# Optimization experiments

Measured on AMD Instinct MI355X. Metric: run time of the kernel, lower is better.

The kernel has to match this reference:

```python
import jax, jax.numpy as jnp
import numpy as np

# Each of the 16 soft binary logic functions f_i(a,b) used by difflogic's
# LogicLayer is multilinear in {1, a, b, a*b}. Row i gives coefficients
# (c1, ca, cb, cab) such that f_i(a,b) = c1 + ca*a + cb*b + cab*a*b.
LOGIC_COEFFS = jnp.array([
    [0.,  0.,  0.,  0.],   # 0: False
    [0.,  0.,  0.,  1.],   # 1: a AND b
    [0.,  1.,  0., -1.],   # 2: a AND NOT b
    [0.,  1.,  0.,  0.],   # 3: a
    [0.,  0.,  1., -1.],   # 4: NOT a AND b
    [0.,  0.,  1.,  0.],   # 5: b
    [0.,  1.,  1., -2.],   # 6: a XOR b
    [0.,  1.,  1., -1.],   # 7: a OR b
    [1., -1., -1.,  1.],   # 8: NOT (a OR b)
    [1., -1., -1.,  2.],   # 9: NOT (a XOR b)
    [1.,  0., -1.,  0.],   # 10: NOT b
    [1.,  0., -1.,  1.],   # 11: a OR NOT b
    [1., -1.,  0.,  0.],   # 12: NOT a
    [1., -1.,  0.,  1.],   # 13: NOT a OR b
    [1.,  0.,  0., -1.],   # 14: NOT (a AND b)
    [1.,  0.,  0.,  0.],   # 15: True
], dtype=jnp.float32)

BATCH = 8192
K = 4096          # num_neurons
L = 6             # num_layers (1 layer 2->K, then L-1 layers K->K)
CLASS_COUNT = 2
TAU = 1.0


def _logic_layer(h, idx, w):
    # h: [B, in_dim], idx: [2, K] int, w: [K, 16]
    a = jnp.take(h, idx[0], axis=1)             # [B, K]
    b = jnp.take(h, idx[1], axis=1)             # [B, K]
    c = jax.nn.softmax(w, axis=-1) @ LOGIC_COEFFS  # [K, 4]
    return c[:, 0] + c[:, 1] * a + c[:, 2] * b + c[:, 3] * (a * b)


def setup_inputs() -> dict:
    key = jax.random.key(0)
    k1, k2, k3, k4, k5 = jax.random.split(key, 5)
    x = jax.random.normal(k1, (BATCH, 2), dtype=jnp.float32)
    w0 = jax.random.normal(k2, (K, 16), dtype=jnp.float32)
    ws = jax.random.normal(k3, (L - 1, K, 16), dtype=jnp.float32)
    idx0 = jax.random.randint(k4, (2, K), 0, 2, dtype=jnp.int32)
    idxs = jax.random.randint(k5, (L - 1, 2, K), 0, K, dtype=jnp.int32)
    return {"x": x, "w0": w0, "ws": ws, "idx0": idx0, "idxs": idxs}


def reference(x, w0, ws, idx0, idxs):
    h = (x > 0.0).astype(jnp.float32)            # binarize input
    h = _logic_layer(h, idx0, w0)                # 2 -> K

    def step(h, wi):
        w, idx = wi
        return _logic_layer(h, idx, w), None

    h, _ = jax.lax.scan(step, h, (ws, idxs))     # (L-1) layers K -> K
    B, Kd = h.shape
    # GroupSum(class_count=2, tau=1.0)
    return h.reshape(B, CLASS_COUNT, Kd // CLASS_COUNT).sum(-1) / TAU
```

## Files before the change

kernel.cpp:

```cpp
#include <hip/hip_runtime.h>

#define KN    4096
#define LTOT  6
#define BATCH 8192
#define NT    1024
#define NITER (KN / NT)
#define NPAT  4

#if __has_builtin(__builtin_amdgcn_cvt_pk_u8_f32)
#define CVT_PK_U8(o, r, enc) __builtin_amdgcn_cvt_pk_u8_f32((o), (r), (enc))
#else
#define CVT_PK_U8(o, r, enc) ((enc) | ((unsigned)(int)(o) << (8 * (r))))
#endif

__global__ __launch_bounds__(256) void pack_kernel(const float* __restrict__ w0,
                                                   const float* __restrict__ ws,
                                                   const int* __restrict__ idx0,
                                                   const int* __restrict__ idxs,
                                                   uint2* __restrict__ pk) {
    const float TAB[16][4] = {
        {0.f, 0.f, 0.f, 0.f}, {0.f, 0.f, 0.f, 1.f}, {0.f, 1.f, 0.f,-1.f}, {0.f, 1.f, 0.f, 0.f},
        {0.f, 0.f, 1.f,-1.f}, {0.f, 0.f, 1.f, 0.f}, {0.f, 1.f, 1.f,-2.f}, {0.f, 1.f, 1.f,-1.f},
        {1.f,-1.f,-1.f, 1.f}, {1.f,-1.f,-1.f, 2.f}, {1.f, 0.f,-1.f, 0.f}, {1.f, 0.f,-1.f, 1.f},
        {1.f,-1.f, 0.f, 0.f}, {1.f,-1.f, 0.f, 1.f}, {1.f, 0.f, 0.f,-1.f}, {1.f, 0.f, 0.f, 0.f}
    };
    int gid = blockIdx.x * 256 + threadIdx.x;
    if (gid >= LTOT * KN) return;
    int l = gid >> 12;
    int k = gid & (KN - 1);
    const float* w = (l == 0) ? (w0 + k * 16) : (ws + ((size_t)((l - 1) * KN + k) << 4));
    float wv[16];
    float m = -1e30f;
#pragma unroll
    for (int j = 0; j < 16; ++j) { wv[j] = w[j]; m = fmaxf(m, wv[j]); }
    float s = 0.f;
#pragma unroll
    for (int j = 0; j < 16; ++j) { wv[j] = __expf(wv[j] - m); s += wv[j]; }
    float inv = 1.0f / s;
    float c0 = 0.f, c1 = 0.f, c2 = 0.f, c3 = 0.f;
#pragma unroll
    for (int j = 0; j < 16; ++j) {
        c0 += wv[j] * TAB[j][0];
        c1 += wv[j] * TAB[j][1];
        c2 += wv[j] * TAB[j][2];
        c3 += wv[j] * TAB[j][3];
    }
    c0 *= inv; c1 *= inv; c2 *= inv; c3 *= inv;

    float w00 = c0;
    float w01 = c0 + c2;
    float w10 = c0 + c1;
    float w11 = c0 + c1 + c2 + c3;
    unsigned q00 = (unsigned)min(255, max(0, (int)(w00 * 255.f + 0.5f)));
    unsigned q01 = (unsigned)min(255, max(0, (int)(w01 * 255.f + 0.5f)));
    unsigned q10 = (unsigned)min(255, max(0, (int)(w10 * 255.f + 0.5f)));
    unsigned q11 = (unsigned)min(255, max(0, (int)(w11 * 255.f + 0.5f)));

    int ia, ib;
    if (l == 0) { ia = idx0[k];                            ib = idx0[KN + k]; }
    else        { ia = idxs[(size_t)(l - 1) * 2 * KN + k]; ib = idxs[(size_t)(l - 1) * 2 * KN + KN + k]; }

    uint2 e;
    e.x = ((unsigned)ia * 4u) | (((unsigned)ib * 4u) << 16);
    e.y = q00 | (q01 << 8) | (q10 << 16) | (q11 << 24);
    pk[gid] = e;
}

#define COEFFS(CW)                                                              \
    float W00 = (float)((CW) & 0xffu);                                          \
    float W01 = (float)(((CW) >> 8) & 0xffu);                                   \
    float W10 = (float)(((CW) >> 16) & 0xffu);                                  \
    float W11 = (float)((CW) >> 24);                                            \
    float C1  = W00 + 0.5f;                                                     \
    float CA  = (W10 - W00) * (1.f / 255.f);                                    \
    float CB  = (W01 - W00) * (1.f / 255.f);                                    \
    float CAB = (W11 - W10 - W01 + W00) * (1.f / 65025.f);

__global__ __launch_bounds__(NT) void net_kernel(const uint2* __restrict__ pk,
                                                 float* __restrict__ table) {
    __shared__ unsigned hbuf[2][KN];
    __shared__ float red[NT / 64][8];

    const int t = threadIdx.x;

    uint2 op[LTOT][NITER];
#pragma unroll
    for (int l = 0; l < LTOT; ++l)
#pragma unroll
        for (int i = 0; i < NITER; ++i)
            op[l][i] = pk[(size_t)l * KN + i * NT + t];

#pragma unroll
    for (int l = 0; l < LTOT; ++l)
#pragma unroll
        for (int i = 0; i < NITER; ++i)
            asm volatile("" :: "v"(op[l][i].x), "v"(op[l][i].y));

#pragma unroll
    for (int i = 0; i < NITER; ++i) {
        int k = t + i * NT;
        unsigned px = op[0][i].x;
        unsigned av = (px & 0xffffu) ? 0xFFFF0000u : 0xFF00FF00u;
        unsigned bv = (px >> 16)     ? 0xFFFF0000u : 0xFF00FF00u;
        COEFFS(op[0][i].y);
        unsigned enc = 0;
#pragma unroll
        for (int r = 0; r < 4; ++r) {
            float af = (float)((av >> (8 * r)) & 0xffu);
            float bf = (float)((bv >> (8 * r)) & 0xffu);
            float o = fmaf(fmaf(CAB, bf, CA), af, fmaf(CB, bf, C1));
            enc = CVT_PK_U8(o, r, enc);
        }
        hbuf[0][k] = enc;
    }
    __syncthreads();

#pragma unroll
    for (int l = 1; l <= 4; ++l) {
        const char* hs = (const char*)&hbuf[(l + 1) & 1][0];
        unsigned*   hd = &hbuf[l & 1][0];
#pragma unroll
        for (int i = 0; i < NITER; ++i) {
            int k = t + i * NT;
            unsigned px = op[l][i].x;
            unsigned av = *(const unsigned*)(hs + (px & 0xffffu));
            unsigned bv = *(const unsigned*)(hs + (px >> 16));
            COEFFS(op[l][i].y);
            unsigned enc = 0;
#pragma unroll
            for (int r = 0; r < 4; ++r) {
                float af = (float)((av >> (8 * r)) & 0xffu);
                float bf = (float)((bv >> (8 * r)) & 0xffu);
                float o = fmaf(fmaf(CAB, bf, CA), af, fmaf(CB, bf, C1));
                enc = CVT_PK_U8(o, r, enc);
            }
            hd[k] = enc;
        }
        __syncthreads();
    }

    float acc[8];
#pragma unroll
    for (int j = 0; j < 8; ++j) acc[j] = 0.f;
    {
        const char* hs = (const char*)&hbuf[0][0];
#pragma unroll
        for (int i = 0; i < NITER; ++i) {
            unsigned px = op[5][i].x;
            unsigned av = *(const unsigned*)(hs + (px & 0xffffu));
            unsigned bv = *(const unsigned*)(hs + (px >> 16));
            COEFFS(op[5][i].y);
            const int cls = (i >= 2) ? 1 : 0;
#pragma unroll
            for (int r = 0; r < 4; ++r) {
                float af = (float)((av >> (8 * r)) & 0xffu);
                float bf = (float)((bv >> (8 * r)) & 0xffu);
                acc[r * 2 + cls] += fmaf(fmaf(CAB, bf, CA), af, fmaf(CB, bf, C1));
            }
        }
    }
#pragma unroll
    for (int j = 0; j < 8; ++j)
#pragma unroll
        for (int off = 32; off > 0; off >>= 1)
            acc[j] += __shfl_down(acc[j], off);
    int wave = t >> 6, lane = t & 63;
    if (lane == 0) {
#pragma unroll
        for (int j = 0; j < 8; ++j) red[wave][j] = acc[j];
    }
    __syncthreads();
    if (t < 8) {
        float s = 0.f;
#pragma unroll
        for (int w = 0; w < NT / 64; ++w) s += red[w][t];
        table[t] = (s - 1024.0f) * (1.0f / 255.0f);
    }
}

__global__ __launch_bounds__(256) void scatter_kernel(const float* __restrict__ x,
                                                      const float* __restrict__ table,
                                                      float2* __restrict__ out) {
    int b = blockIdx.x * 256 + threadIdx.x;
    float2 xv = ((const float2*)x)[b];
    int pat = (xv.x > 0.f ? 1 : 0) | (xv.y > 0.f ? 2 : 0);
    out[b] = ((const float2*)table)[pat];
}

extern "C" void kernel_launch(void* const* d_in, const int* in_sizes, int n_in,
                              void* d_out, int out_size, void* d_ws, size_t ws_size,
                              hipStream_t stream) {
    const float* x    = (const float*)d_in[0];
    const float* w0   = (const float*)d_in[1];
    const float* ws   = (const float*)d_in[2];
    const int*   idx0 = (const int*)d_in[3];
    const int*   idxs = (const int*)d_in[4];
    float*       out  = (float*)d_out;

    uint2* pk    = (uint2*)d_ws;
    float* table = (float*)((char*)d_ws + LTOT * KN * 8);

    pack_kernel<<<(LTOT * KN + 255) / 256, 256, 0, stream>>>(w0, ws, idx0, idxs, pk);
    net_kernel<<<1, NT, 0, stream>>>(pk, table);
    scatter_kernel<<<BATCH / 256, 256, 0, stream>>>(x, table, (float2*)out);
}
```

Baseline: 21.96 us.

## Split single-block network kernel into per-layer multi-block kernels with atomic group sums

```diff
diff --git a/kernel.cpp b/kernel.cpp
--- a/kernel.cpp
+++ b/kernel.cpp
@@ -3,8 +3,6 @@
 #define KN    4096
 #define LTOT  6
 #define BATCH 8192
-#define NT    1024
-#define NITER (KN / NT)
 #define NPAT  4
 
 #if __has_builtin(__builtin_amdgcn_cvt_pk_u8_f32)
@@ -13,11 +11,23 @@
 #define CVT_PK_U8(o, r, enc) ((enc) | ((unsigned)(int)(o) << (8 * (r))))
 #endif
 
+#define COEFFS(CW)                                                              \
+    float W00 = (float)((CW) & 0xffu);                                          \
+    float W01 = (float)(((CW) >> 8) & 0xffu);                                   \
+    float W10 = (float)(((CW) >> 16) & 0xffu);                                  \
+    float W11 = (float)((CW) >> 24);                                            \
+    float C1  = W00 + 0.5f;                                                     \
+    float CA  = (W10 - W00) * (1.f / 255.f);                                    \
+    float CB  = (W01 - W00) * (1.f / 255.f);                                    \
+    float CAB = (W11 - W10 - W01 + W00) * (1.f / 65025.f);
+
 __global__ __launch_bounds__(256) void pack_kernel(const float* __restrict__ w0,
                                                    const float* __restrict__ ws,
                                                    const int* __restrict__ idx0,
                                                    const int* __restrict__ idxs,
-                                                   uint2* __restrict__ pk) {
+                                                   uint2* __restrict__ pk,
+                                                   unsigned* __restrict__ tbl0,
+                                                   unsigned* __restrict__ gsum) {
     const float TAB[16][4] = {
         {0.f, 0.f, 0.f, 0.f}, {0.f, 0.f, 0.f, 1.f}, {0.f, 1.f, 0.f,-1.f}, {0.f, 1.f, 0.f, 0.f},
         {0.f, 0.f, 1.f,-1.f}, {0.f, 0.f, 1.f, 0.f}, {0.f, 1.f, 1.f,-2.f}, {0.f, 1.f, 1.f,-1.f},
@@ -26,6 +36,7 @@
     };
     int gid = blockIdx.x * 256 + threadIdx.x;
     if (gid >= LTOT * KN) return;
+    if (gid < 8) gsum[gid] = 0u;
     int l = gid >> 12;
     int k = gid & (KN - 1);
     const float* w = (l == 0) ? (w0 + k * 16) : (ws + ((size_t)((l - 1) * KN + k) << 4));
@@ -60,131 +71,83 @@
     if (l == 0) { ia = idx0[k];                            ib = idx0[KN + k]; }
     else        { ia = idxs[(size_t)(l - 1) * 2 * KN + k]; ib = idxs[(size_t)(l - 1) * 2 * KN + KN + k]; }
 
-    uint2 e;
-    e.x = ((unsigned)ia * 4u) | (((unsigned)ib * 4u) << 16);
-    e.y = q00 | (q01 << 8) | (q10 << 16) | (q11 << 24);
-    pk[gid] = e;
+    if (l == 0) {
+        unsigned enc = 0;
+#pragma unroll
+        for (int p = 0; p < 4; ++p) {
+            unsigned a = (ia ? (p >> 1) : p) & 1;
+            unsigned b = (ib ? (p >> 1) : p) & 1;
+            unsigned q = a ? (b ? q11 : q10) : (b ? q01 : q00);
+            enc |= q << (8 * p);
+        }
+        tbl0[k] = enc;
+    } else {
+        uint2 e;
+        e.x = ((unsigned)ia * 4u) | (((unsigned)ib * 4u) << 16);
+        e.y = q00 | (q01 << 8) | (q10 << 16) | (q11 << 24);
+        pk[(size_t)(l - 1) * KN + k] = e;
+    }
 }
 
-#define COEFFS(CW)                                                              \
-    float W00 = (float)((CW) & 0xffu);                                          \
-    float W01 = (float)(((CW) >> 8) & 0xffu);                                   \
-    float W10 = (float)(((CW) >> 16) & 0xffu);                                  \
-    float W11 = (float)((CW) >> 24);                                            \
-    float C1  = W00 + 0.5f;                                                     \
-    float CA  = (W10 - W00) * (1.f / 255.f);                                    \
-    float CB  = (W01 - W00) * (1.f / 255.f);                                    \
-    float CAB = (W11 - W10 - W01 + W00) * (1.f / 65025.f);
+__global__ __launch_bounds__(128) void layer_kernel(const uint2* __restrict__ rec,
+                                                    const unsigned* __restrict__ tin,
+                                                    unsigned* __restrict__ tout) {
+    int k = blockIdx.x * 128 + threadIdx.x;
+    uint2 e = rec[k];
+    unsigned av = *(const unsigned*)((const char*)tin + (e.x & 0xffffu));
+    unsigned bv = *(const unsigned*)((const char*)tin + (e.x >> 16));
+    COEFFS(e.y);
+    unsigned enc = 0;
+#pragma unroll
+    for (int r = 0; r < 4; ++r) {
+        float af = (float)((av >> (8 * r)) & 0xffu);
+        float bf = (float)((bv >> (8 * r)) & 0xffu);
+        float o = fmaf(fmaf(CAB, bf, CA), af, fmaf(CB, bf, C1));
+        enc = CVT_PK_U8(o, r, enc);
+    }
+    tout[k] = enc;
+}
 
-__global__ __launch_bounds__(NT) void net_kernel(const uint2* __restrict__ pk,
-                                                 float* __restrict__ table) {
-    __shared__ unsigned hbuf[2][KN];
-    __shared__ float red[NT / 64][8];
-
-    const int t = threadIdx.x;
-
-    uint2 op[LTOT][NITER];
+__global__ __launch_bounds__(128) void layer5_kernel(const uint2* __restrict__ rec,
+                                                     const unsigned* __restrict__ tin,
+                                                     unsigned* __restrict__ gsum) {
+    int k = blockIdx.x * 128 + threadIdx.x;
+    uint2 e = rec[k];
+    unsigned av = *(const unsigned*)((const char*)tin + (e.x & 0xffffu));
+    unsigned bv = *(const unsigned*)((const char*)tin + (e.x >> 16));
+    COEFFS(e.y);
+    unsigned enc = 0;
 #pragma unroll
-    for (int l = 0; l < LTOT; ++l)
+    for (int r = 0; r < 4; ++r) {
+        float af = (float)((av >> (8 * r)) & 0xffu);
+        float bf = (float)((bv >> (8 * r)) & 0xffu);
+        float o = fmaf(fmaf(CAB, bf, CA), af, fmaf(CB, bf, C1));
+        enc = CVT_PK_U8(o, r, enc);
+    }
+    const int cls = (k >= KN / 2) ? 1 : 0;
+    unsigned q[4];
 #pragma unroll
-        for (int i = 0; i < NITER; ++i)
-            op[l][i] = pk[(size_t)l * KN + i * NT + t];
-
+    for (int r = 0; r < 4; ++r) q[r] = (enc >> (8 * r)) & 0xffu;
 #pragma unroll
-    for (int l = 0; l < LTOT; ++l)
-#pragma unroll
-        for (int i = 0; i < NITER; ++i)
-            asm volatile("" :: "v"(op[l][i].x), "v"(op[l][i].y));
-
-#pragma unroll
-    for (int i = 0; i < NITER; ++i) {
-        int k = t + i * NT;
-        unsigned px = op[0][i].x;
-        unsigned av = (px & 0xffffu) ? 0xFFFF0000u : 0xFF00FF00u;
-        unsigned bv = (px >> 16)     ? 0xFFFF0000u : 0xFF00FF00u;
-        COEFFS(op[0][i].y);
-        unsigned enc = 0;
-#pragma unroll
-        for (int r = 0; r < 4; ++r) {
-            float af = (float)((av >> (8 * r)) & 0xffu);
-            float bf = (float)((bv >> (8 * r)) & 0xffu);
-            float o = fmaf(fmaf(CAB, bf, CA), af, fmaf(CB, bf, C1));
-            enc = CVT_PK_U8(o, r, enc);
-        }
-        hbuf[0][k] = enc;
-    }
-    __syncthreads();
-
-#pragma unroll
-    for (int l = 1; l <= 4; ++l) {
-        const char* hs = (const char*)&hbuf[(l + 1) & 1][0];
-        unsigned*   hd = &hbuf[l & 1][0];
-#pragma unroll
-        for (int i = 0; i < NITER; ++i) {
-            int k = t + i * NT;
-            unsigned px = op[l][i].x;
-            unsigned av = *(const unsigned*)(hs + (px & 0xffffu));
-            unsigned bv = *(const unsigned*)(hs + (px >> 16));
-            COEFFS(op[l][i].y);
-            unsigned enc = 0;
-#pragma unroll
-            for (int r = 0; r < 4; ++r) {
-                float af = (float)((av >> (8 * r)) & 0xffu);
-                float bf = (float)((bv >> (8 * r)) & 0xffu);
-                float o = fmaf(fmaf(CAB, bf, CA), af, fmaf(CB, bf, C1));
-                enc = CVT_PK_U8(o, r, enc);
-            }
-            hd[k] = enc;
-        }
-        __syncthreads();
-    }
-
-    float acc[8];
-#pragma unroll
-    for (int j = 0; j < 8; ++j) acc[j] = 0.f;
-    {
-        const char* hs = (const char*)&hbuf[0][0];
-#pragma unroll
-        for (int i = 0; i < NITER; ++i) {
-            unsigned px = op[5][i].x;
-            unsigned av = *(const unsigned*)(hs + (px & 0xffffu));
-            unsigned bv = *(const unsigned*)(hs + (px >> 16));
-            COEFFS(op[5][i].y);
-            const int cls = (i >= 2) ? 1 : 0;
-#pragma unroll
-            for (int r = 0; r < 4; ++r) {
-                float af = (float)((av >> (8 * r)) & 0xffu);
-                float bf = (float)((bv >> (8 * r)) & 0xffu);
-                acc[r * 2 + cls] += fmaf(fmaf(CAB, bf, CA), af, fmaf(CB, bf, C1));
-            }
-        }
-    }
-#pragma unroll
-    for (int j = 0; j < 8; ++j)
+    for (int r = 0; r < 4; ++r)
 #pragma unroll
         for (int off = 32; off > 0; off >>= 1)
-            acc[j] += __shfl_down(acc[j], off);
-    int wave = t >> 6, lane = t & 63;
-    if (lane == 0) {
+            q[r] += __shfl_down(q[r], off);
+    if ((threadIdx.x & 63) == 0) {
 #pragma unroll
-        for (int j = 0; j < 8; ++j) red[wave][j] = acc[j];
-    }
-    __syncthreads();
-    if (t < 8) {
-        float s = 0.f;
-#pragma unroll
-        for (int w = 0; w < NT / 64; ++w) s += red[w][t];
-        table[t] = (s - 1024.0f) * (1.0f / 255.0f);
+        for (int r = 0; r < 4; ++r)
+            atomicAdd(&gsum[r * 2 + cls], q[r]);
     }
 }
 
 __global__ __launch_bounds__(256) void scatter_kernel(const float* __restrict__ x,
-                                                      const float* __restrict__ table,
+                                                      const unsigned* __restrict__ gsum,
                                                       float2* __restrict__ out) {
     int b = blockIdx.x * 256 + threadIdx.x;
     float2 xv = ((const float2*)x)[b];
     int pat = (xv.x > 0.f ? 1 : 0) | (xv.y > 0.f ? 2 : 0);
-    out[b] = ((const float2*)table)[pat];
+    out[b] = make_float2((float)gsum[pat * 2 + 0] * (1.f / 255.f),
+                         (float)gsum[pat * 2 + 1] * (1.f / 255.f));
 }
 
 extern "C" void kernel_launch(void* const* d_in, const int* in_sizes, int n_in,
@@ -197,10 +160,17 @@
     const int*   idxs = (const int*)d_in[4];
     float*       out  = (float*)d_out;
 
-    uint2* pk    = (uint2*)d_ws;
-    float* table = (float*)((char*)d_ws + LTOT * KN * 8);
+    uint2*    pk   = (uint2*)d_ws;
+    unsigned* tbl0 = (unsigned*)((char*)d_ws + 5 * KN * 8);
+    unsigned* tbl1 = tbl0 + KN;
+    unsigned* gsum = tbl1 + KN;
 
-    pack_kernel<<<(LTOT * KN + 255) / 256, 256, 0, stream>>>(w0, ws, idx0, idxs, pk);
-    net_kernel<<<1, NT, 0, stream>>>(pk, table);
-    scatter_kernel<<<BATCH / 256, 256, 0, stream>>>(x, table, (float2*)out);
+    pack_kernel<<<(LTOT * KN + 255) / 256, 256, 0, stream>>>(w0, ws, idx0, idxs,
+                                                             pk, tbl0, gsum);
+    layer_kernel<<<KN / 128, 128, 0, stream>>>(pk + 0 * KN, tbl0, tbl1);
+    layer_kernel<<<KN / 128, 128, 0, stream>>>(pk + 1 * KN, tbl1, tbl0);
+    layer_kernel<<<KN / 128, 128, 0, stream>>>(pk + 2 * KN, tbl0, tbl1);
+    layer_kernel<<<KN / 128, 128, 0, stream>>>(pk + 3 * KN, tbl1, tbl0);
+    layer5_kernel<<<KN / 128, 128, 0, stream>>>(pk + 4 * KN, tbl0, gsum);
+    scatter_kernel<<<BATCH / 256, 256, 0, stream>>>(x, gsum, (float2*)out);
 }
```

New measurement: 23.59 us. 1.07x slower.
